# Kernel optimization log

Measured on AMD Instinct MI355X. Metric: run time of the kernel, lower is better.

The kernel has to match this reference:

```python
import jax, jax.numpy as jnp
import numpy as np

B, N = 4096, 128
STATE_DIM, GOAL_DIM, OBSTACLE_DIM = 6, 6, 4
VEH = 2 * STATE_DIM + GOAL_DIM  # 18


def setup_inputs() -> dict:
    key = jax.random.key(0)
    ks = jax.random.split(key, 8)
    s = lambda k, shp, fan: jax.random.normal(k, shp, jnp.float32) / np.sqrt(fan)
    return {
        "obs": jax.random.normal(ks[0], (B, 138), jnp.float32),
        "obstacles": jax.random.uniform(ks[1], (B, 5, N), jnp.float32),
        "act": jax.random.normal(ks[2], (B, 2), jnp.float32),
        "ow1": s(ks[3], (22, 256), 22),
        "ob1": jnp.zeros((256,), jnp.float32),
        "ow2": s(ks[4], (256, 256), 256),
        "ob2": jnp.zeros((256,), jnp.float32),
        "qw1": s(ks[5], (396, 256), 396),
        "qb1": jnp.zeros((256,), jnp.float32),
        "qw2": s(ks[6], (256, 256), 256),
        "qb2": jnp.zeros((256,), jnp.float32),
        "qw3": s(ks[7], (256, 1), 256),
        "qb3": jnp.zeros((1,), jnp.float32),
    }


def reference(obs, obstacles, act, ow1, ob1, ow2, ob2, qw1, qb1, qw2, qb2, qw3, qb3):
    # obs: [B, 138]; obstacles: [B, obstacle_dim+1, N]; act: [B, 2]
    veh = obs[:, :VEH]                                 # [B, 18]
    obst_data = obstacles[:, :OBSTACLE_DIM, :]         # [B, 4, N]
    mask = obstacles[:, -1, :]                         # [B, N]
    # per-obstacle features: concat broadcast vehicle state with obstacle data -> [B, N, 22]
    x = jnp.concatenate(
        [jnp.broadcast_to(veh[:, None, :], (veh.shape[0], obst_data.shape[2], VEH)),
         obst_data.transpose(0, 2, 1)], axis=-1)
    # shared obstacle MLP (ReLU on both layers, incl. output_activation)
    h = jax.nn.relu(jnp.einsum("bnf,fh->bnh", x, ow1) + ob1)
    h = jax.nn.relu(jnp.einsum("bnh,hk->bnk", h, ow2) + ob2)  # [B, N, 256]
    # masked sum-pool over obstacle axis
    pooled = jnp.einsum("bnh,bn->bh", h, mask)         # [B, 256]
    comb = jnp.concatenate([obs, pooled, act], axis=-1)  # [B, 396]
    q = jax.nn.relu(comb @ qw1 + qb1)
    q = jax.nn.relu(q @ qw2 + qb2)
    q = q @ qw3 + qb3                                   # [B, 1]
    return jnp.squeeze(q, -1)
```

## Files before the change

kernel.cpp:

```cpp
#include <hip/hip_runtime.h>
#include <hip/hip_bf16.h>


typedef __attribute__((ext_vector_type(8))) short short8;
typedef __attribute__((ext_vector_type(4))) float f32x4;

#define MFMA16(A, B, C) __builtin_amdgcn_mfma_f32_16x16x32_bf16(A, B, C, 0, 0, 0)

__device__ __forceinline__ unsigned short f2b(float f) {
  __hip_bfloat16 h = __float2bfloat16(f);
  return __builtin_bit_cast(unsigned short, h);
}
__device__ __forceinline__ float b2f(unsigned short u) {
  unsigned v = ((unsigned)u) << 16;
  return __builtin_bit_cast(float, v);
}
__device__ __forceinline__ unsigned pk2f(float a, float b) {
  unsigned ua = __builtin_bit_cast(unsigned, a) + 0x8000u;
  unsigned ub = __builtin_bit_cast(unsigned, b) + 0x8000u;
  return __builtin_amdgcn_perm(ub, ua, 0x07060302u);
}

__global__ __launch_bounds__(256) void pack_weights(
    const float* __restrict__ ow1, const float* __restrict__ ow2,
    const float* __restrict__ qw1, const float* __restrict__ qw2,
    unsigned short* __restrict__ ow1q, unsigned short* __restrict__ ow2p,
    unsigned short* __restrict__ qw1h, unsigned short* __restrict__ qw1l,
    unsigned short* __restrict__ qw2h, unsigned short* __restrict__ qw2l) {
  int i = blockIdx.x * 256 + threadIdx.x;
  if (i < 8192) {
    int j = i & 7;
    int l15 = (i >> 3) & 15;
    int quad = (i >> 7) & 3;
    int mt = (i >> 9) & 15;
    int k = quad * 8 + j;
    float v = (k < 22) ? ow1[k * 256 + (mt * 16 + l15)] : 0.f;
    ow1q[i] = f2b(v);
  }
  if (i < 65536) {
    int j = i & 7;
    int n = (i >> 3) & 255;
    int qq = i >> 11;
    int k = (qq >> 2) * 32 + (qq & 3) * 8 + j;
    ow2p[i] = f2b(ow2[k * 256 + n]);
    float w = qw2[k * 256 + n];
    unsigned short h = f2b(w);
    qw2h[i] = h;
    qw2l[i] = f2b(w - b2f(h));
  }
  if (i < 106496) {
    int j = i & 7;
    int n = (i >> 3) & 255;
    int qq = i >> 11;
    int k = (qq >> 2) * 32 + (qq & 3) * 8 + j;
    float w = (k < 396) ? qw1[k * 256 + n] : 0.f;
    unsigned short h = f2b(w);
    qw1h[i] = h;
    qw1l[i] = f2b(w - b2f(h));
  }
}

#define XSTR 40
#define HSTR 264

__global__ __launch_bounds__(512, 4) void obstacle_kernel(
    const float* __restrict__ obs, const float* __restrict__ obstacles,
    const unsigned short* __restrict__ ow1q,
    const unsigned short* __restrict__ ow2p,
    const float* __restrict__ ob1, const float* __restrict__ ob2,
    unsigned short* __restrict__ poolH, unsigned short* __restrict__ poolL) {
  __shared__ unsigned short xs[128 * XSTR];
  __shared__ unsigned short h1[128 * HSTR];
  __shared__ float maskS[128];
  __shared__ unsigned short vehB[32];

  const int b = blockIdx.x;
  const int tid = threadIdx.x;

  if (tid < 18) vehB[tid] = f2b(obs[b * 138 + tid]);
  if (tid < 128) maskS[tid] = obstacles[b * 640 + 512 + tid];
  __syncthreads();

  if (tid < 256) {
    int n = tid >> 1;
    int half = tid & 1;
    unsigned short* wr = &xs[n * XSTR + half * 16];
    if (half == 0) {
      unsigned short r01[16];
#pragma unroll
      for (int k = 0; k < 16; k++) r01[k] = vehB[k];
      *(short8*)(wr + 0) = *(short8*)&r01[0];
      *(short8*)(wr + 8) = *(short8*)&r01[8];
    } else {
      unsigned short r2[8];
      r2[0] = vehB[16];
      r2[1] = vehB[17];
#pragma unroll
      for (int d = 0; d < 4; d++)
        r2[2 + d] = f2b(obstacles[b * 640 + d * 128 + n]);
      r2[6] = 0; r2[7] = 0;
      *(short8*)(wr + 0) = *(short8*)&r2[0];
      short8 z = {0, 0, 0, 0, 0, 0, 0, 0};
      *(short8*)(wr + 8) = z;
    }
  }
  __syncthreads();

  const int wave = tid >> 6;
  const int lane = tid & 63;
  const int quad = lane >> 4;
  const int l15 = lane & 15;

  {
    const unsigned short* wp = &ow1q[wave * 1024 + quad * 128 + l15 * 8];
    short8 wfr[2];
#pragma unroll
    for (int i = 0; i < 2; i++) wfr[i] = *(const short8*)(wp + i * 512);

    const unsigned short* bxp = &xs[l15 * XSTR + quad * 8];
    short8 bx[8];
#pragma unroll
    for (int nt = 0; nt < 8; nt++)
      bx[nt] = *(const short8*)(bxp + nt * 16 * XSTR);

    unsigned short* wrb = &h1[l15 * HSTR + wave * 32 + quad * 4];

#pragma unroll
    for (int i = 0; i < 2; i++) {
      f32x4 cinit = *(const f32x4*)&ob1[wave * 32 + i * 16 + quad * 4];
      f32x4 acc1[8];
#pragma unroll
      for (int nt = 0; nt < 8; nt++) acc1[nt] = MFMA16(wfr[i], bx[nt], cinit);
#pragma unroll
      for (int nt = 0; nt < 8; nt++) {
        float v0 = fmaxf(acc1[nt][0], 0.f);
        float v1 = fmaxf(acc1[nt][1], 0.f);
        float v2 = fmaxf(acc1[nt][2], 0.f);
        float v3 = fmaxf(acc1[nt][3], 0.f);
        uint2 pk;
        pk.x = pk2f(v0, v1);
        pk.y = pk2f(v2, v3);
        *(uint2*)(wrb + nt * 16 * HSTR + i * 16) = pk;
      }
    }
  }
  __syncthreads();

  f32x4 acc[8][2];
#pragma unroll
  for (int t = 0; t < 2; t++) {
    float bv = ob2[wave * 32 + t * 16 + l15];
    f32x4 bvec = {bv, bv, bv, bv};
#pragma unroll
    for (int mt = 0; mt < 8; mt++) acc[mt][t] = bvec;
  }

  const unsigned short* bp = &ow2p[(quad * 256 + wave * 32 + l15) * 8];
  const unsigned short* h1r = &h1[l15 * HSTR + quad * 8];
  short8 bcur[2], bnxt[2];
#pragma unroll
  for (int t = 0; t < 2; t++) bcur[t] = *(const short8*)(bp + t * 128);

#pragma unroll 1
  for (int kb = 0; kb < 8; kb++) {
    if (kb < 7) {
#pragma unroll
      for (int t = 0; t < 2; t++)
        bnxt[t] = *(const short8*)(bp + 8192 + t * 128);
    }
    short8 afr[8];
#pragma unroll
    for (int mt = 0; mt < 8; mt++)
      afr[mt] = *(const short8*)(h1r + mt * 16 * HSTR);
#pragma unroll
    for (int mt = 0; mt < 8; mt++)
#pragma unroll
      for (int t = 0; t < 2; t++) acc[mt][t] = MFMA16(afr[mt], bcur[t], acc[mt][t]);
    bp += 8192;
    h1r += 32;
    if (kb < 7) {
#pragma unroll
      for (int t = 0; t < 2; t++) bcur[t] = bnxt[t];
    }
  }

  f32x4 mk[8];
  const float* mkp = &maskS[quad * 4];
#pragma unroll
  for (int mt = 0; mt < 8; mt++) mk[mt] = *(const f32x4*)(mkp + mt * 16);

#pragma unroll
  for (int t = 0; t < 2; t++) {
    float s = 0.f;
#pragma unroll
    for (int mt = 0; mt < 8; mt++) {
#pragma unroll
      for (int r = 0; r < 4; r++) {
        float v = fmaxf(acc[mt][t][r], 0.f);
        s = fmaf(mk[mt][r], v, s);
      }
    }
    s += __shfl_xor(s, 16);
    s += __shfl_xor(s, 32);
    if (quad == 0) {
      int n = wave * 32 + t * 16 + l15;
      unsigned short sh = (unsigned short)(__builtin_bit_cast(unsigned, s) >> 16);
      poolH[b * 256 + n] = sh;
      poolL[b * 256 + n] = f2b(s - b2f(sh));
    }
  }
}

__global__ __launch_bounds__(1024) void head_mfma(
    const float* __restrict__ obs, const float* __restrict__ act,
    const unsigned short* __restrict__ poolH,
    const unsigned short* __restrict__ poolL,
    const unsigned short* __restrict__ qw1h,
    const unsigned short* __restrict__ qw1l,
    const unsigned short* __restrict__ qw2h,
    const unsigned short* __restrict__ qw2l,
    const float* __restrict__ qb1, const float* __restrict__ qb2,
    const float* __restrict__ qw3, const float* __restrict__ qb3,
    float* __restrict__ out) {
  const int CSTR = 424;
  const int HSTRQ = 264;
  __shared__ unsigned short combH[16 * 424], combL[16 * 424];
  __shared__ unsigned short h1H[16 * 264], h1L[16 * 264];
  __shared__ float wred[16][16];

  const int tid = threadIdx.x;
  const int r0 = blockIdx.x * 16;

  for (int idx = tid; idx < 16 * 416; idx += 1024) {
    int m = idx / 416;
    int k = idx - m * 416;
    unsigned short hi, lo;
    if (k < 138) {
      float v = obs[(r0 + m) * 138 + k];
      hi = f2b(v);
      lo = f2b(v - b2f(hi));
    } else if (k < 394) {
      hi = poolH[(r0 + m) * 256 + (k - 138)];
      lo = poolL[(r0 + m) * 256 + (k - 138)];
    } else if (k < 396) {
      float v = act[(r0 + m) * 2 + (k - 394)];
      hi = f2b(v);
      lo = f2b(v - b2f(hi));
    } else {
      hi = 0; lo = 0;
    }
    combH[m * CSTR + k] = hi;
    combL[m * CSTR + k] = lo;
  }
  __syncthreads();

  const int wave = tid >> 6;
  const int lane = tid & 63;
  const int quad = lane >> 4;
  const int l15 = lane & 15;
  const int n = wave * 16 + l15;

  f32x4 acc = {0.f, 0.f, 0.f, 0.f}, accm = {0.f, 0.f, 0.f, 0.f};
#pragma unroll 1
  for (int kb = 0; kb < 13; kb++) {
    int ao = l15 * CSTR + kb * 32 + quad * 8;
    short8 ah = *(const short8*)&combH[ao];
    short8 al = *(const short8*)&combL[ao];
    int off = ((kb * 4 + quad) * 256 + n) * 8;
    short8 bh = *(const short8*)&qw1h[off];
    short8 bl = *(const short8*)&qw1l[off];
    acc = MFMA16(ah, bh, acc);
    accm = MFMA16(ah, bl, accm);
    accm = MFMA16(al, bh, accm);
  }
  {
    float bias = qb1[n];
#pragma unroll
    for (int r = 0; r < 4; r++) {
      int m = quad * 4 + r;
      float v = fmaxf(acc[r] + accm[r] + bias, 0.f);
      unsigned short hi = f2b(v);
      h1H[m * HSTRQ + n] = hi;
      h1L[m * HSTRQ + n] = f2b(v - b2f(hi));
    }
  }
  __syncthreads();

  f32x4 a2 = {0.f, 0.f, 0.f, 0.f}, a2m = {0.f, 0.f, 0.f, 0.f};
#pragma unroll 1
  for (int kb = 0; kb < 8; kb++) {
    int ao = l15 * HSTRQ + kb * 32 + quad * 8;
    short8 ah = *(const short8*)&h1H[ao];
    short8 al = *(const short8*)&h1L[ao];
    int off = ((kb * 4 + quad) * 256 + n) * 8;
    short8 bh = *(const short8*)&qw2h[off];
    short8 bl = *(const short8*)&qw2l[off];
    a2 = MFMA16(ah, bh, a2);
    a2m = MFMA16(ah, bl, a2m);
    a2m = MFMA16(al, bh, a2m);
  }

  {
    float w3 = qw3[n];
    float qb2n = qb2[n];
#pragma unroll
    for (int r = 0; r < 4; r++) {
      float v = fmaxf(a2[r] + a2m[r] + qb2n, 0.f);
      float s = v * w3;
      s += __shfl_xor(s, 1);
      s += __shfl_xor(s, 2);
      s += __shfl_xor(s, 4);
      s += __shfl_xor(s, 8);
      if (l15 == 0) wred[wave][quad * 4 + r] = s;
    }
  }
  __syncthreads();
  if (tid < 16) {
    float s = qb3[0];
#pragma unroll
    for (int w = 0; w < 16; w++) s += wred[w][tid];
    out[r0 + tid] = s;
  }
}

extern "C" void kernel_launch(void* const* d_in, const int* in_sizes, int n_in,
                              void* d_out, int out_size, void* d_ws, size_t ws_size,
                              hipStream_t stream) {
  const float* obs       = (const float*)d_in[0];
  const float* obstacles = (const float*)d_in[1];
  const float* act       = (const float*)d_in[2];
  const float* ow1       = (const float*)d_in[3];
  const float* ob1       = (const float*)d_in[4];
  const float* ow2       = (const float*)d_in[5];
  const float* ob2       = (const float*)d_in[6];
  const float* qw1       = (const float*)d_in[7];
  const float* qb1       = (const float*)d_in[8];
  const float* qw2       = (const float*)d_in[9];
  const float* qb2       = (const float*)d_in[10];
  const float* qw3       = (const float*)d_in[11];
  const float* qb3       = (const float*)d_in[12];
  float* out = (float*)d_out;

  unsigned short* ow1q = (unsigned short*)d_ws;
  unsigned short* ow2p = ow1q + 8192;
  unsigned short* qw1h = ow2p + 65536;
  unsigned short* qw1l = qw1h + 106496;
  unsigned short* qw2h = qw1l + 106496;
  unsigned short* qw2l = qw2h + 65536;
  unsigned short* poolH = qw2l + 65536;
  unsigned short* poolL = poolH + 1048576;

  pack_weights<<<416, 256, 0, stream>>>(ow1, ow2, qw1, qw2, ow1q, ow2p, qw1h,
                                        qw1l, qw2h, qw2l);
  obstacle_kernel<<<4096, 512, 0, stream>>>(obs, obstacles, ow1q, ow2p, ob1,
                                            ob2, poolH, poolL);
  head_mfma<<<256, 1024, 0, stream>>>(obs, act, poolH, poolL, qw1h, qw1l,
                                      qw2h, qw2l, qb1, qb2, qw3, qb3, out);
}
```

Measured before the change: 166.8 us.

## Switch obstacle layer-2 GEMM to 32x32 MFMA with 4-wave blocks

The second obstacle MLP layer now uses 32x32x16 bf16 MFMA tiles instead of 16x16x32, and the ow2 weights are repacked into the matching layout. Each block shrinks from 8 to 4 waves, so every wave covers 64 output columns in both layers. The larger tiles should raise arithmetic per LDS fragment load and halve the number of weight fragments fetched per output, at the cost of more accumulator registers and fewer waves per block to hide latency. The pooled reduction and mask indexing are rewritten for the 32x32 accumulator layout.

```diff
diff --git a/kernel.cpp b/kernel.cpp
--- a/kernel.cpp
+++ b/kernel.cpp
@@ -4,8 +4,10 @@
 
 typedef __attribute__((ext_vector_type(8))) short short8;
 typedef __attribute__((ext_vector_type(4))) float f32x4;
+typedef __attribute__((ext_vector_type(16))) float f32x16;
 
 #define MFMA16(A, B, C) __builtin_amdgcn_mfma_f32_16x16x32_bf16(A, B, C, 0, 0, 0)
+#define MFMA32(A, B, C) __builtin_amdgcn_mfma_f32_32x32x16_bf16(A, B, C, 0, 0, 0)
 
 __device__ __forceinline__ unsigned short f2b(float f) {
   __hip_bfloat16 h = __float2bfloat16(f);
@@ -24,7 +26,7 @@
 __global__ __launch_bounds__(256) void pack_weights(
     const float* __restrict__ ow1, const float* __restrict__ ow2,
     const float* __restrict__ qw1, const float* __restrict__ qw2,
-    unsigned short* __restrict__ ow1q, unsigned short* __restrict__ ow2p,
+    unsigned short* __restrict__ ow1q, unsigned short* __restrict__ ow2q,
     unsigned short* __restrict__ qw1h, unsigned short* __restrict__ qw1l,
     unsigned short* __restrict__ qw2h, unsigned short* __restrict__ qw2l) {
   int i = blockIdx.x * 256 + threadIdx.x;
@@ -40,9 +42,12 @@
   if (i < 65536) {
     int j = i & 7;
     int n = (i >> 3) & 255;
+    int hh = (i >> 11) & 1;
+    int ks = i >> 12;
+    int k32 = ks * 16 + hh * 8 + j;
+    ow2q[i] = f2b(ow2[k32 * 256 + n]);
     int qq = i >> 11;
     int k = (qq >> 2) * 32 + (qq & 3) * 8 + j;
-    ow2p[i] = f2b(ow2[k * 256 + n]);
     float w = qw2[k * 256 + n];
     unsigned short h = f2b(w);
     qw2h[i] = h;
@@ -63,10 +68,10 @@
 #define XSTR 40
 #define HSTR 264
 
-__global__ __launch_bounds__(512, 4) void obstacle_kernel(
+__global__ __launch_bounds__(256, 2) void obstacle_kernel(
     const float* __restrict__ obs, const float* __restrict__ obstacles,
     const unsigned short* __restrict__ ow1q,
-    const unsigned short* __restrict__ ow2p,
+    const unsigned short* __restrict__ ow2q,
     const float* __restrict__ ob1, const float* __restrict__ ob2,
     unsigned short* __restrict__ poolH, unsigned short* __restrict__ poolL) {
   __shared__ unsigned short xs[128 * XSTR];
@@ -81,7 +86,7 @@
   if (tid < 128) maskS[tid] = obstacles[b * 640 + 512 + tid];
   __syncthreads();
 
-  if (tid < 256) {
+  {
     int n = tid >> 1;
     int half = tid & 1;
     unsigned short* wr = &xs[n * XSTR + half * 16];
@@ -112,10 +117,10 @@
   const int l15 = lane & 15;
 
   {
-    const unsigned short* wp = &ow1q[wave * 1024 + quad * 128 + l15 * 8];
-    short8 wfr[2];
-#pragma unroll
-    for (int i = 0; i < 2; i++) wfr[i] = *(const short8*)(wp + i * 512);
+    const unsigned short* wp = &ow1q[wave * 2048 + quad * 128 + l15 * 8];
+    short8 wfr[4];
+#pragma unroll
+    for (int i = 0; i < 4; i++) wfr[i] = *(const short8*)(wp + i * 512);
 
     const unsigned short* bxp = &xs[l15 * XSTR + quad * 8];
     short8 bx[8];
@@ -123,11 +128,11 @@
     for (int nt = 0; nt < 8; nt++)
       bx[nt] = *(const short8*)(bxp + nt * 16 * XSTR);
 
-    unsigned short* wrb = &h1[l15 * HSTR + wave * 32 + quad * 4];
-
-#pragma unroll
-    for (int i = 0; i < 2; i++) {
-      f32x4 cinit = *(const f32x4*)&ob1[wave * 32 + i * 16 + quad * 4];
+    unsigned short* wrb = &h1[l15 * HSTR + wave * 64 + quad * 4];
+
+#pragma unroll
+    for (int i = 0; i < 4; i++) {
+      f32x4 cinit = *(const f32x4*)&ob1[wave * 64 + i * 16 + quad * 4];
       f32x4 acc1[8];
 #pragma unroll
       for (int nt = 0; nt < 8; nt++) acc1[nt] = MFMA16(wfr[i], bx[nt], cinit);
@@ -146,64 +151,72 @@
   }
   __syncthreads();
 
-  f32x4 acc[8][2];
+  const int h32 = lane >> 5;
+  const int l31 = lane & 31;
+
+  f32x16 acc[4][2];
 #pragma unroll
   for (int t = 0; t < 2; t++) {
-    float bv = ob2[wave * 32 + t * 16 + l15];
-    f32x4 bvec = {bv, bv, bv, bv};
-#pragma unroll
-    for (int mt = 0; mt < 8; mt++) acc[mt][t] = bvec;
-  }
-
-  const unsigned short* bp = &ow2p[(quad * 256 + wave * 32 + l15) * 8];
-  const unsigned short* h1r = &h1[l15 * HSTR + quad * 8];
+    float bv = ob2[(wave * 2 + t) * 32 + l31];
+#pragma unroll
+    for (int mt = 0; mt < 4; mt++)
+#pragma unroll
+      for (int r = 0; r < 16; r++) acc[mt][t][r] = bv;
+  }
+
+  const unsigned short* bp = &ow2q[(h32 * 256 + wave * 64 + l31) * 8];
+  const unsigned short* h1r = &h1[l31 * HSTR + h32 * 8];
   short8 bcur[2], bnxt[2];
 #pragma unroll
-  for (int t = 0; t < 2; t++) bcur[t] = *(const short8*)(bp + t * 128);
+  for (int t = 0; t < 2; t++) bcur[t] = *(const short8*)(bp + t * 256);
 
 #pragma unroll 1
-  for (int kb = 0; kb < 8; kb++) {
-    if (kb < 7) {
+  for (int ks = 0; ks < 16; ks++) {
+    if (ks < 15) {
 #pragma unroll
       for (int t = 0; t < 2; t++)
-        bnxt[t] = *(const short8*)(bp + 8192 + t * 128);
-    }
-    short8 afr[8];
-#pragma unroll
-    for (int mt = 0; mt < 8; mt++)
-      afr[mt] = *(const short8*)(h1r + mt * 16 * HSTR);
-#pragma unroll
-    for (int mt = 0; mt < 8; mt++)
-#pragma unroll
-      for (int t = 0; t < 2; t++) acc[mt][t] = MFMA16(afr[mt], bcur[t], acc[mt][t]);
-    bp += 8192;
-    h1r += 32;
-    if (kb < 7) {
+        bnxt[t] = *(const short8*)(bp + 4096 + t * 256);
+    }
+    short8 afr[4];
+#pragma unroll
+    for (int mt = 0; mt < 4; mt++)
+      afr[mt] = *(const short8*)(h1r + mt * 32 * HSTR);
+#pragma unroll
+    for (int mt = 0; mt < 4; mt++)
+#pragma unroll
+      for (int t = 0; t < 2; t++) acc[mt][t] = MFMA32(afr[mt], bcur[t], acc[mt][t]);
+    bp += 4096;
+    h1r += 16;
+    if (ks < 15) {
 #pragma unroll
       for (int t = 0; t < 2; t++) bcur[t] = bnxt[t];
     }
   }
 
-  f32x4 mk[8];
-  const float* mkp = &maskS[quad * 4];
-#pragma unroll
-  for (int mt = 0; mt < 8; mt++) mk[mt] = *(const f32x4*)(mkp + mt * 16);
+  f32x4 mk[4][4];
+#pragma unroll
+  for (int mt = 0; mt < 4; mt++)
+#pragma unroll
+    for (int g = 0; g < 4; g++)
+      mk[mt][g] = *(const f32x4*)&maskS[mt * 32 + g * 8 + h32 * 4];
 
 #pragma unroll
   for (int t = 0; t < 2; t++) {
     float s = 0.f;
 #pragma unroll
-    for (int mt = 0; mt < 8; mt++) {
-#pragma unroll
-      for (int r = 0; r < 4; r++) {
-        float v = fmaxf(acc[mt][t][r], 0.f);
-        s = fmaf(mk[mt][r], v, s);
+    for (int mt = 0; mt < 4; mt++) {
+#pragma unroll
+      for (int g = 0; g < 4; g++) {
+#pragma unroll
+        for (int j = 0; j < 4; j++) {
+          float v = fmaxf(acc[mt][t][g * 4 + j], 0.f);
+          s = fmaf(mk[mt][g][j], v, s);
+        }
       }
     }
-    s += __shfl_xor(s, 16);
     s += __shfl_xor(s, 32);
-    if (quad == 0) {
-      int n = wave * 32 + t * 16 + l15;
+    if (h32 == 0) {
+      int n = (wave * 2 + t) * 32 + l31;
       unsigned short sh = (unsigned short)(__builtin_bit_cast(unsigned, s) >> 16);
       poolH[b * 256 + n] = sh;
       poolL[b * 256 + n] = f2b(s - b2f(sh));
@@ -342,17 +355,17 @@
   float* out = (float*)d_out;
 
   unsigned short* ow1q = (unsigned short*)d_ws;
-  unsigned short* ow2p = ow1q + 8192;
-  unsigned short* qw1h = ow2p + 65536;
+  unsigned short* ow2q = ow1q + 8192;
+  unsigned short* qw1h = ow2q + 65536;
   unsigned short* qw1l = qw1h + 106496;
   unsigned short* qw2h = qw1l + 106496;
   unsigned short* qw2l = qw2h + 65536;
   unsigned short* poolH = qw2l + 65536;
   unsigned short* poolL = poolH + 1048576;
 
-  pack_weights<<<416, 256, 0, stream>>>(ow1, ow2, qw1, qw2, ow1q, ow2p, qw1h,
+  pack_weights<<<416, 256, 0, stream>>>(ow1, ow2, qw1, qw2, ow1q, ow2q, qw1h,
                                         qw1l, qw2h, qw2l);
-  obstacle_kernel<<<4096, 512, 0, stream>>>(obs, obstacles, ow1q, ow2p, ob1,
+  obstacle_kernel<<<4096, 256, 0, stream>>>(obs, obstacles, ow1q, ow2q, ob1,
                                             ob2, poolH, poolL);
   head_mfma<<<256, 1024, 0, stream>>>(obs, act, poolH, poolL, qw1h, qw1l,
                                       qw2h, qw2l, qb1, qb2, qw3, qb3, out);
```

New measurement: 173.9 us. 1.04x slower.
